# Performance work log

Measured on AMD Instinct MI355X. Metric: run time of the kernel, lower is better.

## Reference

```python
import jax, jax.numpy as jnp
import numpy as np

N_NODES = 50000   # gates in the circuit batch
N_HOPS = 100000   # number of k-hop cones
MAX_PI = 8        # max PIs per hop (padded, masked via stats == -1)
D = 128           # token_emb / hidden
D_FF = 4 * D      # cls_head hidden width (512)
TT = 64           # max_tt_len -> logits width
LN_EPS = 1e-5


def setup_inputs() -> dict:
    key = jax.random.key(0)
    ks = jax.random.split(key, 8)
    hf = jax.random.normal(ks[0], (N_NODES, D), jnp.float32)
    all_hop_pi = jax.random.randint(ks[1], (N_HOPS, MAX_PI), 0, N_NODES)
    # stats in {-1, 0, 1}; -1 marks an invalid (padded) PI slot
    all_hop_pi_stats = jax.random.randint(ks[2], (N_HOPS, MAX_PI), 0, 3) - 1
    all_hop_po = jax.random.randint(ks[3], (N_HOPS,), 0, N_NODES)
    w_q = jax.random.normal(ks[4], (D,), jnp.float32) / np.sqrt(D)
    W1 = jax.random.normal(ks[5], (D, D_FF), jnp.float32) / np.sqrt(D)
    b1 = jnp.zeros((D_FF,), jnp.float32)
    gamma = jnp.ones((D_FF,), jnp.float32)
    beta = jnp.zeros((D_FF,), jnp.float32)
    W2 = jax.random.normal(ks[6], (D_FF, TT), jnp.float32) / np.sqrt(D_FF)
    b2 = jnp.zeros((TT,), jnp.float32)
    return {
        'hf': hf, 'w_q': w_q, 'W1': W1, 'b1': b1, 'gamma': gamma,
        'beta': beta, 'W2': W2, 'b2': b2,
        'all_hop_pi': all_hop_pi, 'all_hop_pi_stats': all_hop_pi_stats,
        'all_hop_po': all_hop_po,
    }


def reference(hf, w_q, W1, b1, gamma, beta, W2, b2,
              all_hop_pi, all_hop_pi_stats, all_hop_po):
    # Per-hop gather: valid PI embeddings + PO embedding -> [H, P+1, D]
    pi_tok = hf[all_hop_pi]                       # [H, P, D]
    po_tok = hf[all_hop_po][:, None, :]           # [H, 1, D]
    tokens = jnp.concatenate([pi_tok, po_tok], axis=1)
    valid = jnp.concatenate(
        [all_hop_pi_stats != -1,
         jnp.ones((all_hop_po.shape[0], 1), bool)], axis=1)  # [H, P+1]
    # tf_Pooling: masked single-query attention pooling over the ragged set
    scores = jnp.einsum('hpd,d->hp', tokens, w_q) / jnp.sqrt(jnp.float32(D))
    scores = jnp.where(valid, scores, jnp.float32(-1e30))
    attn = jax.nn.softmax(scores, axis=-1)
    hop_hf = jnp.einsum('hp,hpd->hd', attn, tokens)  # [H, D]
    # cls_head: Linear(D, 4D) -> ReLU -> LayerNorm(4D) -> Linear(4D, TT)
    h = jax.nn.relu(hop_hf @ W1 + b1)
    mu = jnp.mean(h, axis=-1, keepdims=True)
    var = jnp.var(h, axis=-1, keepdims=True)
    h = (h - mu) * jax.lax.rsqrt(var + LN_EPS) * gamma + beta
    logits = h @ W2 + b2                           # [H, TT]
    return logits
```

## Files before the change

kernel.cpp:

```cpp
#include <hip/hip_runtime.h>
#include <math.h>

#define DIM 128
#define DFF 512
#define TTW 64
#define NPI 8
#define NTOK 9
#define POOL_HOPS 16
#define HEAD_HOPS 32

typedef __attribute__((ext_vector_type(8))) short short8;
typedef __attribute__((ext_vector_type(4))) float float4v;

__device__ __forceinline__ unsigned short f32_bf16(float f) {
    union { float f; unsigned u; } v; v.f = f;
    unsigned r = v.u + 0x7FFFu + ((v.u >> 16) & 1u);
    return (unsigned short)(r >> 16);
}
__device__ __forceinline__ float bf16_f32(unsigned short h) {
    union { unsigned u; float f; } v; v.u = (unsigned)h << 16;
    return v.f;
}

__global__ __launch_bounds__(256)
void prep_k(const float* __restrict__ hf, const float* __restrict__ W1,
            const float* __restrict__ W2, const int* __restrict__ pi,
            const int* __restrict__ stats,
            unsigned short* __restrict__ hf2, unsigned short* __restrict__ w1t,
            unsigned short* __restrict__ w2t, int* __restrict__ cpack,
            int n_hf, int B_HF, int n_pk)
{
    __shared__ float tile[32][33];
    const int b = blockIdx.x, t = threadIdx.x;
    if (b < B_HF) {
        int i = (b * 256 + t) * 4;
        if (i < n_hf) {
            float4v v = *(const float4v*)(hf + i);
            unsigned long long p =  (unsigned long long)f32_bf16(v[0])
                                 | ((unsigned long long)f32_bf16(v[1]) << 16)
                                 | ((unsigned long long)f32_bf16(v[2]) << 32)
                                 | ((unsigned long long)f32_bf16(v[3]) << 48);
            *(unsigned long long*)(hf2 + i) = p;
        }
    } else if (b < B_HF + 64) {
        const int tb = b - B_HF;
        const int r0 = (tb & 3) * 32, c0 = (tb >> 2) * 32;
        const int ty = t >> 3, tx = t & 7;
        *(float4v*)&tile[ty][tx * 4] = *(const float4v*)(W1 + (r0 + ty) * DFF + c0 + tx * 4);
        __syncthreads();
        unsigned long long p = 0;
        #pragma unroll
        for (int j = 0; j < 4; ++j)
            p |= (unsigned long long)f32_bf16(tile[tx * 4 + j][ty]) << (16 * j);
        *(unsigned long long*)(w1t + (c0 + ty) * DIM + r0 + tx * 4) = p;
    } else if (b < B_HF + 96) {
        const int tb = b - B_HF - 64;
        const int r0 = (tb & 15) * 32, c0 = (tb >> 4) * 32;
        const int ty = t >> 3, tx = t & 7;
        *(float4v*)&tile[ty][tx * 4] = *(const float4v*)(W2 + (r0 + ty) * TTW + c0 + tx * 4);
        __syncthreads();
        unsigned long long p = 0;
        #pragma unroll
        for (int j = 0; j < 4; ++j)
            p |= (unsigned long long)f32_bf16(tile[tx * 4 + j][ty]) << (16 * j);
        *(unsigned long long*)(w2t + (c0 + ty) * DFF + r0 + tx * 4) = p;
    } else {
        const int pb = b - (B_HF + 96);
        int i = (pb * 256 + t) * 4;
        if (i < n_pk) {
            int4 p = *(const int4*)(pi + i);
            int4 s = *(const int4*)(stats + i);
            int4 o;
            o.x = p.x | (s.x == -1 ? (int)0x80000000 : 0);
            o.y = p.y | (s.y == -1 ? (int)0x80000000 : 0);
            o.z = p.z | (s.z == -1 ? (int)0x80000000 : 0);
            o.w = p.w | (s.w == -1 ? (int)0x80000000 : 0);
            *(int4*)(cpack + i) = o;
        }
    }
}

__global__ __launch_bounds__(256, 4)
void pool_k(const unsigned short* __restrict__ hf2,
            const float* __restrict__ w_q,
            const int* __restrict__ cpack,
            const int* __restrict__ po,
            unsigned short* __restrict__ pooled,
            int H)
{
    const int t = threadIdx.x;
    const int g = t >> 4, l = t & 15;
    const int hop = blockIdx.x * POOL_HOPS + g;
    if (hop >= H) return;

    float wq[8];
    {
        float4v a = *(const float4v*)(w_q + l * 8);
        float4v b = *(const float4v*)(w_q + l * 8 + 4);
        wq[0]=a[0]; wq[1]=a[1]; wq[2]=a[2]; wq[3]=a[3];
        wq[4]=b[0]; wq[5]=b[1]; wq[6]=b[2]; wq[7]=b[3];
    }
    int idx[NTOK]; bool val[NTOK];
    {
        int4 c0 = *(const int4*)(cpack + hop * NPI);
        int4 c1 = *(const int4*)(cpack + hop * NPI + 4);
        idx[0]=c0.x & 0x7fffffff; val[0]=c0.x >= 0;
        idx[1]=c0.y & 0x7fffffff; val[1]=c0.y >= 0;
        idx[2]=c0.z & 0x7fffffff; val[2]=c0.z >= 0;
        idx[3]=c0.w & 0x7fffffff; val[3]=c0.w >= 0;
        idx[4]=c1.x & 0x7fffffff; val[4]=c1.x >= 0;
        idx[5]=c1.y & 0x7fffffff; val[5]=c1.y >= 0;
        idx[6]=c1.z & 0x7fffffff; val[6]=c1.z >= 0;
        idx[7]=c1.w & 0x7fffffff; val[7]=c1.w >= 0;
        idx[8]=po[hop]; val[8]=true;
    }
    short8 tok[NTOK];
    #pragma unroll
    for (int p = 0; p < NTOK; ++p)
        tok[p] = *(const short8*)(hf2 + (size_t)idx[p] * DIM + l * 8);

    float sc[NTOK];
    #pragma unroll
    for (int p = 0; p < NTOK; ++p) {
        float s = 0.f;
        #pragma unroll
        for (int j = 0; j < 8; ++j)
            s += bf16_f32((unsigned short)tok[p][j]) * wq[j];
        sc[p] = s;
    }
    #pragma unroll
    for (int m = 1; m < 16; m <<= 1) {
        #pragma unroll
        for (int p = 0; p < NTOK; ++p) sc[p] += __shfl_xor(sc[p], m);
    }
    const float isd = 0.08838834764831845f;
    float mx = -1e30f;
    #pragma unroll
    for (int p = 0; p < NTOK; ++p) {
        sc[p] = val[p] ? sc[p] * isd : -1e30f;
        mx = fmaxf(mx, sc[p]);
    }
    float se = 0.f;
    #pragma unroll
    for (int p = 0; p < NTOK; ++p) { sc[p] = __expf(sc[p] - mx); se += sc[p]; }
    const float inv = 1.f / se;
    float acc[8] = {0,0,0,0,0,0,0,0};
    #pragma unroll
    for (int p = 0; p < NTOK; ++p) {
        float a = sc[p] * inv;
        #pragma unroll
        for (int j = 0; j < 8; ++j)
            acc[j] += a * bf16_f32((unsigned short)tok[p][j]);
    }
    unsigned long long p0 = 0, p1 = 0;
    #pragma unroll
    for (int j = 0; j < 4; ++j) p0 |= (unsigned long long)f32_bf16(acc[j])     << (16 * j);
    #pragma unroll
    for (int j = 0; j < 4; ++j) p1 |= (unsigned long long)f32_bf16(acc[4 + j]) << (16 * j);
    unsigned long long* dst = (unsigned long long*)(pooled + (size_t)hop * DIM + l * 8);
    dst[0] = p0; dst[1] = p1;
}

__global__ __launch_bounds__(256, 3)
void head_k(const unsigned short* __restrict__ pooled,
            const unsigned short* __restrict__ w1t,
            const float* __restrict__ b1,
            const float* __restrict__ gamma,
            const float* __restrict__ beta,
            const unsigned short* __restrict__ w2t,
            const float* __restrict__ b2,
            float* __restrict__ out,
            int H)
{
    __shared__ unsigned short Hsm[HEAD_HOPS][DFF + 8];

    const int t    = threadIdx.x;
    const int lane = t & 63;
    const int w    = t >> 6;
    const int row  = lane & 15;
    const int quad = lane >> 4;
    const int hop0 = blockIdx.x * HEAD_HOPS;

    {
        short8 bfr[2][4];
        #pragma unroll
        for (int ks = 0; ks < 4; ++ks) {
            const int k0 = ks * 32 + quad * 8;
            #pragma unroll
            for (int ht = 0; ht < 2; ++ht) {
                int hp = hop0 + ht * 16 + row;
                if (hp >= H) hp = H - 1;
                bfr[ht][ks] = *(const short8*)(pooled + (size_t)hp * DIM + k0);
            }
        }
        #pragma unroll
        for (int mt = 0; mt < 8; ++mt) {
            float4v acc0 = (float4v){0.f, 0.f, 0.f, 0.f};
            float4v acc1 = (float4v){0.f, 0.f, 0.f, 0.f};
            const unsigned short* wrow = w1t + (size_t)(w * 128 + mt * 16 + row) * DIM;
            #pragma unroll
            for (int ks = 0; ks < 4; ++ks) {
                short8 afr = *(const short8*)(wrow + ks * 32 + quad * 8);
                acc0 = __builtin_amdgcn_mfma_f32_16x16x32_bf16(afr, bfr[0][ks], acc0, 0, 0, 0);
                acc1 = __builtin_amdgcn_mfma_f32_16x16x32_bf16(afr, bfr[1][ks], acc1, 0, 0, 0);
            }
            const int nb = w * 128 + mt * 16 + quad * 4;
            const float4v bias = *(const float4v*)(b1 + nb);
            unsigned long long p0 = 0, p1 = 0;
            #pragma unroll
            for (int r = 0; r < 4; ++r) {
                float v0 = fmaxf(acc0[r] + bias[r], 0.f);
                float v1 = fmaxf(acc1[r] + bias[r], 0.f);
                p0 |= (unsigned long long)f32_bf16(v0) << (16 * r);
                p1 |= (unsigned long long)f32_bf16(v1) << (16 * r);
            }
            *(unsigned long long*)&Hsm[row][nb]      = p0;
            *(unsigned long long*)&Hsm[16 + row][nb] = p1;
        }
    }
    __syncthreads();

    {
        const int r = t >> 3;
        const int s = t & 7;
        float sum = 0.f, ssq = 0.f;
        #pragma unroll
        for (int k = 0; k < 8; ++k) {
            short8 hv = *(const short8*)&Hsm[r][s * 8 + k * 64];
            #pragma unroll
            for (int e = 0; e < 8; ++e) {
                float v = bf16_f32((unsigned short)hv[e]);
                sum += v; ssq += v * v;
            }
        }
        #pragma unroll
        for (int m = 1; m < 8; m <<= 1) {
            sum += __shfl_xor(sum, m);
            ssq += __shfl_xor(ssq, m);
        }
        const float invn = 1.f / (float)DFF;
        float mu  = sum * invn;
        float var = ssq * invn - mu * mu;
        float rs  = rsqrtf(var + 1e-5f);
        #pragma unroll
        for (int k = 0; k < 8; ++k) {
            const int col = s * 8 + k * 64;
            short8 hv = *(const short8*)&Hsm[r][col];
            float4v g0 = *(const float4v*)(gamma + col);
            float4v g1 = *(const float4v*)(gamma + col + 4);
            float4v be0 = *(const float4v*)(beta + col);
            float4v be1 = *(const float4v*)(beta + col + 4);
            unsigned long long q0 = 0, q1 = 0;
            #pragma unroll
            for (int e = 0; e < 4; ++e) {
                float tg = rs * g0[e];
                float o  = bf16_f32((unsigned short)hv[e]) * tg + (be0[e] - mu * tg);
                q0 |= (unsigned long long)f32_bf16(o) << (16 * e);
            }
            #pragma unroll
            for (int e = 0; e < 4; ++e) {
                float tg = rs * g1[e];
                float o  = bf16_f32((unsigned short)hv[4 + e]) * tg + (be1[e] - mu * tg);
                q1 |= (unsigned long long)f32_bf16(o) << (16 * e);
            }
            *(unsigned long long*)&Hsm[r][col]     = q0;
            *(unsigned long long*)&Hsm[r][col + 4] = q1;
        }
    }
    __syncthreads();

    {
        float4v acc2[2];
        acc2[0] = (float4v){0.f,0.f,0.f,0.f};
        acc2[1] = (float4v){0.f,0.f,0.f,0.f};
        #pragma unroll
        for (int ks = 0; ks < 16; ++ks) {
            const int k0 = ks * 32 + quad * 8;
            short8 bfr = *(const short8*)(w2t + (size_t)(w * 16 + row) * DFF + k0);
            #pragma unroll
            for (int mt = 0; mt < 2; ++mt) {
                short8 afr = *(const short8*)&Hsm[mt * 16 + row][k0];
                acc2[mt] = __builtin_amdgcn_mfma_f32_16x16x32_bf16(
                    afr, bfr, acc2[mt], 0, 0, 0);
            }
        }
        const float bb = b2[w * 16 + row];
        #pragma unroll
        for (int mt = 0; mt < 2; ++mt) {
            #pragma unroll
            for (int r = 0; r < 4; ++r) {
                int hop = hop0 + mt * 16 + quad * 4 + r;
                if (hop < H)
                    out[(size_t)hop * TTW + w * 16 + row] = acc2[mt][r] + bb;
            }
        }
    }
}

extern "C" void kernel_launch(void* const* d_in, const int* in_sizes, int n_in,
                              void* d_out, int out_size, void* d_ws, size_t ws_size,
                              hipStream_t stream) {
    const float* hf    = (const float*)d_in[0];
    const float* w_q   = (const float*)d_in[1];
    const float* W1    = (const float*)d_in[2];
    const float* b1    = (const float*)d_in[3];
    const float* gamma = (const float*)d_in[4];
    const float* beta  = (const float*)d_in[5];
    const float* W2    = (const float*)d_in[6];
    const float* b2    = (const float*)d_in[7];
    const int* pi      = (const int*)d_in[8];
    const int* stats   = (const int*)d_in[9];
    const int* po      = (const int*)d_in[10];
    float* out         = (float*)d_out;

    const int n_hf = in_sizes[0];
    const int H    = in_sizes[10];
    const int n_pk = H * NPI;
    const int Hpad = ((H + HEAD_HOPS - 1) / HEAD_HOPS) * HEAD_HOPS;

    char* ws = (char*)d_ws;
    unsigned short* w1t    = (unsigned short*)ws;
    unsigned short* w2t    = (unsigned short*)(ws + 131072);
    unsigned short* hf2    = (unsigned short*)(ws + 196608);
    size_t off_cp = 196608 + ((size_t)n_hf * 2 + 255) / 256 * 256;
    int*            cpack  = (int*)(ws + off_cp);
    size_t off_pl = off_cp + ((size_t)n_pk * 4 + 255) / 256 * 256;
    unsigned short* pooled = (unsigned short*)(ws + off_pl);

    const int B_HF = (n_hf + 1023) / 1024;
    const int B_PK = (n_pk + 1023) / 1024;
    const int prep_blocks = B_HF + 96 + B_PK;

    hipLaunchKernelGGL(prep_k, dim3(prep_blocks), dim3(256), 0, stream,
                       hf, W1, W2, pi, stats, hf2, w1t, w2t, cpack,
                       n_hf, B_HF, n_pk);
    hipLaunchKernelGGL(pool_k, dim3((H + POOL_HOPS - 1) / POOL_HOPS), dim3(256), 0, stream,
                       hf2, w_q, cpack, po, pooled, H);
    hipLaunchKernelGGL(head_k, dim3(Hpad / HEAD_HOPS), dim3(256), 0, stream,
                       pooled, w1t, b1, gamma, beta, w2t, b2, out, H);
}
```

Baseline: 225.8 us.

## Fuse LayerNorm into MFMA epilogue, widen pool lanes, use packed bf16 converts

The head kernel now keeps the first GEMM's accumulators in registers. It computes per-row LayerNorm statistics with shuffles and a small shared-memory partial reduction, then writes normalized bf16 values straight to shared memory. This removes one shared-memory round trip and a separate normalization pass. The pooling kernel uses 32 lanes per hop with 4 elements each (8 hops per block), with higher occupancy bounds and a longer shuffle reduction. Bf16 conversions use packed intrinsics instead of manual bit rounding, and LayerNorm statistics are now taken on fp32 values rather than bf16-rounded ones, so results shift slightly.

```diff
diff --git a/kernel.cpp b/kernel.cpp
--- a/kernel.cpp
+++ b/kernel.cpp
@@ -1,4 +1,5 @@
 #include <hip/hip_runtime.h>
+#include <hip/hip_bf16.h>
 #include <math.h>
 
 #define DIM 128
@@ -6,7 +7,7 @@
 #define TTW 64
 #define NPI 8
 #define NTOK 9
-#define POOL_HOPS 16
+#define POOL_HOPS 8
 #define HEAD_HOPS 32
 
 typedef __attribute__((ext_vector_type(8))) short short8;
@@ -17,9 +18,18 @@
     unsigned r = v.u + 0x7FFFu + ((v.u >> 16) & 1u);
     return (unsigned short)(r >> 16);
 }
-__device__ __forceinline__ float bf16_f32(unsigned short h) {
-    union { unsigned u; float f; } v; v.u = (unsigned)h << 16;
+__device__ __forceinline__ float bf16lo_f32(unsigned u) {
+    union { unsigned u; float f; } v; v.u = u << 16;
     return v.f;
+}
+__device__ __forceinline__ float bf16hi_f32(unsigned u) {
+    union { unsigned u; float f; } v; v.u = u & 0xffff0000u;
+    return v.f;
+}
+__device__ __forceinline__ unsigned pk_bf16(float a, float b) {
+    __hip_bfloat162 h = __float22bfloat162_rn(float2{a, b});
+    union { __hip_bfloat162 h; unsigned u; } cv; cv.h = h;
+    return cv.u;
 }
 
 __global__ __launch_bounds__(256)
@@ -36,11 +46,10 @@
         int i = (b * 256 + t) * 4;
         if (i < n_hf) {
             float4v v = *(const float4v*)(hf + i);
-            unsigned long long p =  (unsigned long long)f32_bf16(v[0])
-                                 | ((unsigned long long)f32_bf16(v[1]) << 16)
-                                 | ((unsigned long long)f32_bf16(v[2]) << 32)
-                                 | ((unsigned long long)f32_bf16(v[3]) << 48);
-            *(unsigned long long*)(hf2 + i) = p;
+            uint2 o;
+            o.x = pk_bf16(v[0], v[1]);
+            o.y = pk_bf16(v[2], v[3]);
+            *(uint2*)(hf2 + i) = o;
         }
     } else if (b < B_HF + 64) {
         const int tb = b - B_HF;
@@ -48,22 +57,20 @@
         const int ty = t >> 3, tx = t & 7;
         *(float4v*)&tile[ty][tx * 4] = *(const float4v*)(W1 + (r0 + ty) * DFF + c0 + tx * 4);
         __syncthreads();
-        unsigned long long p = 0;
-        #pragma unroll
-        for (int j = 0; j < 4; ++j)
-            p |= (unsigned long long)f32_bf16(tile[tx * 4 + j][ty]) << (16 * j);
-        *(unsigned long long*)(w1t + (c0 + ty) * DIM + r0 + tx * 4) = p;
+        uint2 o;
+        o.x = pk_bf16(tile[tx * 4 + 0][ty], tile[tx * 4 + 1][ty]);
+        o.y = pk_bf16(tile[tx * 4 + 2][ty], tile[tx * 4 + 3][ty]);
+        *(uint2*)(w1t + (c0 + ty) * DIM + r0 + tx * 4) = o;
     } else if (b < B_HF + 96) {
         const int tb = b - B_HF - 64;
         const int r0 = (tb & 15) * 32, c0 = (tb >> 4) * 32;
         const int ty = t >> 3, tx = t & 7;
         *(float4v*)&tile[ty][tx * 4] = *(const float4v*)(W2 + (r0 + ty) * TTW + c0 + tx * 4);
         __syncthreads();
-        unsigned long long p = 0;
-        #pragma unroll
-        for (int j = 0; j < 4; ++j)
-            p |= (unsigned long long)f32_bf16(tile[tx * 4 + j][ty]) << (16 * j);
-        *(unsigned long long*)(w2t + (c0 + ty) * DFF + r0 + tx * 4) = p;
+        uint2 o;
+        o.x = pk_bf16(tile[tx * 4 + 0][ty], tile[tx * 4 + 1][ty]);
+        o.y = pk_bf16(tile[tx * 4 + 2][ty], tile[tx * 4 + 3][ty]);
+        *(uint2*)(w2t + (c0 + ty) * DFF + r0 + tx * 4) = o;
     } else {
         const int pb = b - (B_HF + 96);
         int i = (pb * 256 + t) * 4;
@@ -80,7 +87,7 @@
     }
 }
 
-__global__ __launch_bounds__(256, 4)
+__global__ __launch_bounds__(256, 6)
 void pool_k(const unsigned short* __restrict__ hf2,
             const float* __restrict__ w_q,
             const int* __restrict__ cpack,
@@ -89,17 +96,12 @@
             int H)
 {
     const int t = threadIdx.x;
-    const int g = t >> 4, l = t & 15;
+    const int g = t >> 5, l = t & 31;
     const int hop = blockIdx.x * POOL_HOPS + g;
     if (hop >= H) return;
 
-    float wq[8];
-    {
-        float4v a = *(const float4v*)(w_q + l * 8);
-        float4v b = *(const float4v*)(w_q + l * 8 + 4);
-        wq[0]=a[0]; wq[1]=a[1]; wq[2]=a[2]; wq[3]=a[3];
-        wq[4]=b[0]; wq[5]=b[1]; wq[6]=b[2]; wq[7]=b[3];
-    }
+    const float4v wq4 = *(const float4v*)(w_q + l * 4);
+
     int idx[NTOK]; bool val[NTOK];
     {
         int4 c0 = *(const int4*)(cpack + hop * NPI);
@@ -114,22 +116,26 @@
         idx[7]=c1.w & 0x7fffffff; val[7]=c1.w >= 0;
         idx[8]=po[hop]; val[8]=true;
     }
-    short8 tok[NTOK];
+    uint2 tu[NTOK];
     #pragma unroll
     for (int p = 0; p < NTOK; ++p)
-        tok[p] = *(const short8*)(hf2 + (size_t)idx[p] * DIM + l * 8);
-
+        tu[p] = *(const uint2*)(hf2 + (size_t)idx[p] * DIM + l * 4);
+
+    float tok[NTOK][4];
+    #pragma unroll
+    for (int p = 0; p < NTOK; ++p) {
+        tok[p][0] = bf16lo_f32(tu[p].x);
+        tok[p][1] = bf16hi_f32(tu[p].x);
+        tok[p][2] = bf16lo_f32(tu[p].y);
+        tok[p][3] = bf16hi_f32(tu[p].y);
+    }
     float sc[NTOK];
     #pragma unroll
-    for (int p = 0; p < NTOK; ++p) {
-        float s = 0.f;
-        #pragma unroll
-        for (int j = 0; j < 8; ++j)
-            s += bf16_f32((unsigned short)tok[p][j]) * wq[j];
-        sc[p] = s;
-    }
-    #pragma unroll
-    for (int m = 1; m < 16; m <<= 1) {
+    for (int p = 0; p < NTOK; ++p)
+        sc[p] = tok[p][0]*wq4[0] + tok[p][1]*wq4[1]
+              + tok[p][2]*wq4[2] + tok[p][3]*wq4[3];
+    #pragma unroll
+    for (int m = 1; m < 32; m <<= 1) {
         #pragma unroll
         for (int p = 0; p < NTOK; ++p) sc[p] += __shfl_xor(sc[p], m);
     }
@@ -144,21 +150,17 @@
     #pragma unroll
     for (int p = 0; p < NTOK; ++p) { sc[p] = __expf(sc[p] - mx); se += sc[p]; }
     const float inv = 1.f / se;
-    float acc[8] = {0,0,0,0,0,0,0,0};
+    float a0=0.f, a1=0.f, a2=0.f, a3=0.f;
     #pragma unroll
     for (int p = 0; p < NTOK; ++p) {
         float a = sc[p] * inv;
-        #pragma unroll
-        for (int j = 0; j < 8; ++j)
-            acc[j] += a * bf16_f32((unsigned short)tok[p][j]);
-    }
-    unsigned long long p0 = 0, p1 = 0;
-    #pragma unroll
-    for (int j = 0; j < 4; ++j) p0 |= (unsigned long long)f32_bf16(acc[j])     << (16 * j);
-    #pragma unroll
-    for (int j = 0; j < 4; ++j) p1 |= (unsigned long long)f32_bf16(acc[4 + j]) << (16 * j);
-    unsigned long long* dst = (unsigned long long*)(pooled + (size_t)hop * DIM + l * 8);
-    dst[0] = p0; dst[1] = p1;
+        a0 += a * tok[p][0]; a1 += a * tok[p][1];
+        a2 += a * tok[p][2]; a3 += a * tok[p][3];
+    }
+    uint2 o;
+    o.x = pk_bf16(a0, a1);
+    o.y = pk_bf16(a2, a3);
+    *(uint2*)(pooled + (size_t)hop * DIM + l * 4) = o;
 }
 
 __global__ __launch_bounds__(256, 3)
@@ -173,6 +175,7 @@
             int H)
 {
     __shared__ unsigned short Hsm[HEAD_HOPS][DFF + 8];
+    __shared__ float part[2][16][4][2];
 
     const int t    = threadIdx.x;
     const int lane = t & 63;
@@ -181,6 +184,12 @@
     const int quad = lane >> 4;
     const int hop0 = blockIdx.x * HEAD_HOPS;
 
+    float4v acc[8][2];
+    #pragma unroll
+    for (int mt = 0; mt < 8; ++mt) {
+        acc[mt][0] = (float4v){0.f, 0.f, 0.f, 0.f};
+        acc[mt][1] = (float4v){0.f, 0.f, 0.f, 0.f};
+    }
     {
         short8 bfr[2][4];
         #pragma unroll
@@ -195,76 +204,69 @@
         }
         #pragma unroll
         for (int mt = 0; mt < 8; ++mt) {
-            float4v acc0 = (float4v){0.f, 0.f, 0.f, 0.f};
-            float4v acc1 = (float4v){0.f, 0.f, 0.f, 0.f};
             const unsigned short* wrow = w1t + (size_t)(w * 128 + mt * 16 + row) * DIM;
             #pragma unroll
             for (int ks = 0; ks < 4; ++ks) {
                 short8 afr = *(const short8*)(wrow + ks * 32 + quad * 8);
-                acc0 = __builtin_amdgcn_mfma_f32_16x16x32_bf16(afr, bfr[0][ks], acc0, 0, 0, 0);
-                acc1 = __builtin_amdgcn_mfma_f32_16x16x32_bf16(afr, bfr[1][ks], acc1, 0, 0, 0);
-            }
-            const int nb = w * 128 + mt * 16 + quad * 4;
-            const float4v bias = *(const float4v*)(b1 + nb);
-            unsigned long long p0 = 0, p1 = 0;
+                acc[mt][0] = __builtin_amdgcn_mfma_f32_16x16x32_bf16(afr, bfr[0][ks], acc[mt][0], 0, 0, 0);
+                acc[mt][1] = __builtin_amdgcn_mfma_f32_16x16x32_bf16(afr, bfr[1][ks], acc[mt][1], 0, 0, 0);
+            }
+        }
+    }
+    float sum0 = 0.f, ssq0 = 0.f, sum1 = 0.f, ssq1 = 0.f;
+    #pragma unroll
+    for (int mt = 0; mt < 8; ++mt) {
+        const int nb = w * 128 + mt * 16 + quad * 4;
+        const float4v bias = *(const float4v*)(b1 + nb);
+        #pragma unroll
+        for (int r = 0; r < 4; ++r) {
+            float v0 = fmaxf(acc[mt][0][r] + bias[r], 0.f);
+            float v1 = fmaxf(acc[mt][1][r] + bias[r], 0.f);
+            acc[mt][0][r] = v0;  sum0 += v0;  ssq0 += v0 * v0;
+            acc[mt][1][r] = v1;  sum1 += v1;  ssq1 += v1 * v1;
+        }
+    }
+    #pragma unroll
+    for (int m = 16; m <= 32; m <<= 1) {
+        sum0 += __shfl_xor(sum0, m);  ssq0 += __shfl_xor(ssq0, m);
+        sum1 += __shfl_xor(sum1, m);  ssq1 += __shfl_xor(ssq1, m);
+    }
+    if (lane < 16) {
+        part[0][row][w][0] = sum0;  part[0][row][w][1] = ssq0;
+        part[1][row][w][0] = sum1;  part[1][row][w][1] = ssq1;
+    }
+    __syncthreads();
+    float mu[2], rs[2];
+    #pragma unroll
+    for (int ht = 0; ht < 2; ++ht) {
+        float S = 0.f, Q = 0.f;
+        #pragma unroll
+        for (int ww = 0; ww < 4; ++ww) {
+            S += part[ht][row][ww][0];
+            Q += part[ht][row][ww][1];
+        }
+        const float invn = 1.f / (float)DFF;
+        mu[ht] = S * invn;
+        float var = Q * invn - mu[ht] * mu[ht];
+        rs[ht] = rsqrtf(var + 1e-5f);
+    }
+    #pragma unroll
+    for (int mt = 0; mt < 8; ++mt) {
+        const int nb = w * 128 + mt * 16 + quad * 4;
+        const float4v g4  = *(const float4v*)(gamma + nb);
+        const float4v be4 = *(const float4v*)(beta + nb);
+        #pragma unroll
+        for (int ht = 0; ht < 2; ++ht) {
+            float o[4];
             #pragma unroll
             for (int r = 0; r < 4; ++r) {
-                float v0 = fmaxf(acc0[r] + bias[r], 0.f);
-                float v1 = fmaxf(acc1[r] + bias[r], 0.f);
-                p0 |= (unsigned long long)f32_bf16(v0) << (16 * r);
-                p1 |= (unsigned long long)f32_bf16(v1) << (16 * r);
-            }
-            *(unsigned long long*)&Hsm[row][nb]      = p0;
-            *(unsigned long long*)&Hsm[16 + row][nb] = p1;
-        }
-    }
-    __syncthreads();
-
-    {
-        const int r = t >> 3;
-        const int s = t & 7;
-        float sum = 0.f, ssq = 0.f;
-        #pragma unroll
-        for (int k = 0; k < 8; ++k) {
-            short8 hv = *(const short8*)&Hsm[r][s * 8 + k * 64];
-            #pragma unroll
-            for (int e = 0; e < 8; ++e) {
-                float v = bf16_f32((unsigned short)hv[e]);
-                sum += v; ssq += v * v;
-            }
-        }
-        #pragma unroll
-        for (int m = 1; m < 8; m <<= 1) {
-            sum += __shfl_xor(sum, m);
-            ssq += __shfl_xor(ssq, m);
-        }
-        const float invn = 1.f / (float)DFF;
-        float mu  = sum * invn;
-        float var = ssq * invn - mu * mu;
-        float rs  = rsqrtf(var + 1e-5f);
-        #pragma unroll
-        for (int k = 0; k < 8; ++k) {
-            const int col = s * 8 + k * 64;
-            short8 hv = *(const short8*)&Hsm[r][col];
-            float4v g0 = *(const float4v*)(gamma + col);
-            float4v g1 = *(const float4v*)(gamma + col + 4);
-            float4v be0 = *(const float4v*)(beta + col);
-            float4v be1 = *(const float4v*)(beta + col + 4);
-            unsigned long long q0 = 0, q1 = 0;
-            #pragma unroll
-            for (int e = 0; e < 4; ++e) {
-                float tg = rs * g0[e];
-                float o  = bf16_f32((unsigned short)hv[e]) * tg + (be0[e] - mu * tg);
-                q0 |= (unsigned long long)f32_bf16(o) << (16 * e);
-            }
-            #pragma unroll
-            for (int e = 0; e < 4; ++e) {
-                float tg = rs * g1[e];
-                float o  = bf16_f32((unsigned short)hv[4 + e]) * tg + (be1[e] - mu * tg);
-                q1 |= (unsigned long long)f32_bf16(o) << (16 * e);
-            }
-            *(unsigned long long*)&Hsm[r][col]     = q0;
-            *(unsigned long long*)&Hsm[r][col + 4] = q1;
+                float tg = rs[ht] * g4[r];
+                o[r] = acc[mt][ht][r] * tg + (be4[r] - mu[ht] * tg);
+            }
+            uint2 p;
+            p.x = pk_bf16(o[0], o[1]);
+            p.y = pk_bf16(o[2], o[3]);
+            *(uint2*)&Hsm[ht * 16 + row][nb] = p;
         }
     }
     __syncthreads();
```

Result: no change. 225.7 us (-0.0%).
